# Optimization experiments

Hardware: AMD Instinct MI355X
Metric: run time of the kernel (lower is better)

## Reference

```python
import jax, jax.numpy as jnp
import numpy as np

N = 64          # Hilbert space dim
B = 4096        # batch of density matrices
K = 2           # number of jump operators
DT = 0.01       # time step
C = (0.0, 0.5, 1.0)
A = ((0.0, 0.0, 0.0), (0.5, 0.0, 0.0), (0.0, 1.0, 0.0))
BW = (1.0 / 6.0, 2.0 / 3.0, 1.0 / 6.0)
NEUMANN_ORDER = 2


def _dag(M):
    # real-valued reference: dagger == transpose on last two axes
    return jnp.swapaxes(M, -1, -2)


def _sandwich(M, rho):
    # M rho M^dag ; M:[N,N], rho:[B,N,N]
    return M @ rho @ _dag(M)


def _dissipator(L, rho):
    # sum_k L_k rho L_k^dag ; L:[K,N,N], rho:[B,N,N]
    return jnp.einsum('kij,bjl,kml->bim', L, rho, L)


def _neumann_ratio(Ui, Uj, I):
    # U(ci) U(cj)^{-1} with U(cj)^{-1} ~ sum_{p<=order} (I - U(cj))^p
    W = I - Uj
    inv = I
    Wp = I
    for _ in range(NEUMANN_ORDER):
        Wp = Wp @ W
        inv = inv + Wp
    return Ui @ inv


def _forward(rho0, U_half, U_one, L0, Lh, L1):
    I = jnp.eye(N, dtype=rho0.dtype)
    Umap = {0.0: I, 0.5: U_half, 1.0: U_one}
    Lmap = {0.0: L0, 0.5: Lh, 1.0: L1}

    def ratio(ci, cj):
        if ci == cj:
            return I
        if cj == 0.0:
            return Umap[ci]
        return _neumann_ratio(Umap[ci], Umap[cj], I)

    # intermediate stages rho^(i)
    stages = []
    for i, ci in enumerate(C):
        rho_i = rho0 if ci == 0.0 else _sandwich(Umap[ci], rho0)
        for j in range(i):
            a_ij = A[i][j]
            if a_ij == 0.0:
                continue
            cj = C[j]
            P_ij = ratio(ci, cj)
            rho_i = rho_i + DT * a_ij * _sandwich(P_ij, _dissipator(Lmap[cj], stages[j]))
        stages.append(rho_i)

    # output combination
    rho_new = _sandwich(Umap[1.0], rho0)
    for i, bi in enumerate(BW):
        if bi == 0.0:
            continue
        ci = C[i]
        Q_i = ratio(1.0, ci)
        rho_new = rho_new + DT * bi * _sandwich(Q_i, _dissipator(Lmap[ci], stages[i]))
    return rho_new


def setup_inputs() -> dict:
    key = jax.random.key(0)
    k1, k2, k3, k4, k5, k6 = jax.random.split(key, 6)
    I = jnp.eye(N, dtype=jnp.float32)
    rho0 = jax.random.normal(k1, (B, N, N), dtype=jnp.float32)
    rho0 = 0.5 * (rho0 + jnp.swapaxes(rho0, -1, -2))  # hermitian-like
    # no-jump propagators: near-identity so the Neumann series is sane
    U_half = I + 0.02 * jax.random.normal(k2, (N, N), dtype=jnp.float32)
    U_one = I + 0.04 * jax.random.normal(k3, (N, N), dtype=jnp.float32)
    L0 = 0.1 * jax.random.normal(k4, (K, N, N), dtype=jnp.float32)
    Lh = 0.1 * jax.random.normal(k5, (K, N, N), dtype=jnp.float32)
    L1 = 0.1 * jax.random.normal(k6, (K, N, N), dtype=jnp.float32)
    return {"rho0": rho0, "U_half": U_half, "U_one": U_one,
            "L0": L0, "Lh": Lh, "L1": L1}


def reference(rho0, U_half, U_one, L0, Lh, L1):
    return _forward(rho0, U_half, U_one, L0, Lh, L1)
```

## Files before the change

kernel.cpp:

```cpp
#include <hip/hip_runtime.h>
#include <hip/hip_bf16.h>

#define NDIM 64
#define BP   72
#define DT_  0.01f

typedef __attribute__((ext_vector_type(8)))  short bf16x8;
typedef __attribute__((ext_vector_type(16))) float f32x16;

struct Frag { bf16x8 f[4]; };


__device__ __forceinline__ unsigned short f2b(float x) {
    __hip_bfloat16 h = __float2bfloat16(x);
    return __builtin_bit_cast(unsigned short, h);
}
__device__ __forceinline__ float b2f(unsigned short u) {
    unsigned int v = (unsigned int)u << 16;
    return __builtin_bit_cast(float, v);
}
__device__ __forceinline__ unsigned int f2b2(float lo, float hi) {
    return (unsigned int)f2b(lo) | ((unsigned int)f2b(hi) << 16);
}


__device__ __forceinline__ bf16x8 ldfrag(const unsigned short* M, int rb, int j, int ln, int hq) {
    return *(const bf16x8*)&M[(rb + ln) * BP + j * 16 + hq * 8];
}

__device__ __forceinline__ void ldg_op(Frag& F, const unsigned short* __restrict__ p,
                                       int ln, int hq, int cw) {
#pragma unroll
    for (int j = 0; j < 4; ++j)
        F.f[j] = *(const bf16x8*)&p[(cw + ln) * 64 + j * 16 + hq * 8];
}

__device__ __forceinline__ void ldWfrag(Frag& F, const float* __restrict__ Uh,
                                        int ln, int hq, int cw) {
    const int n = cw + ln;
#pragma unroll
    for (int j = 0; j < 4; ++j) {
        const int k0 = j * 16 + hq * 8;
        const float* q = &Uh[n * 64 + k0];
        float4 u = *(const float4*)q;
        float4 v = *(const float4*)(q + 4);
        float wv[8] = {-u.x, -u.y, -u.z, -u.w, -v.x, -v.y, -v.z, -v.w};
#pragma unroll
        for (int e = 0; e < 8; ++e)
            if (n == k0 + e) wv[e] += 1.f;
        uint4 o;
        o.x = f2b2(wv[0], wv[1]); o.y = f2b2(wv[2], wv[3]);
        o.z = f2b2(wv[4], wv[5]); o.w = f2b2(wv[6], wv[7]);
        F.f[j] = __builtin_bit_cast(bf16x8, o);
    }
}

template <bool ACC>
__device__ __forceinline__ void ntg(const unsigned short* A, const Frag& F, f32x16& acc,
                                    int ln, int hq, int rb) {
    if (!ACC) {
#pragma unroll
        for (int r = 0; r < 16; ++r) acc[r] = 0.f;
    }
#pragma unroll
    for (int j = 0; j < 4; ++j)
        acc = __builtin_amdgcn_mfma_f32_32x32x16_bf16(ldfrag(A, rb, j, ln, hq), F.f[j], acc, 0, 0, 0);
}

__device__ __forceinline__ void ntg2(const unsigned short* A, const Frag& Fa, const Frag& Fb,
                                     f32x16& c0, f32x16& c1, int ln, int hq, int rb) {
#pragma unroll
    for (int r = 0; r < 16; ++r) { c0[r] = 0.f; c1[r] = 0.f; }
#pragma unroll
    for (int j = 0; j < 4; ++j) {
        bf16x8 a = ldfrag(A, rb, j, ln, hq);
        c0 = __builtin_amdgcn_mfma_f32_32x32x16_bf16(a, Fa.f[j], c0, 0, 0, 0);
        c1 = __builtin_amdgcn_mfma_f32_32x32x16_bf16(a, Fb.f[j], c1, 0, 0, 0);
    }
}

__device__ __forceinline__ void stT(unsigned short* D, const f32x16& v,
                                    int ln, int hq, int rw, int cw) {
#pragma unroll
    for (int g = 0; g < 4; ++g) {
        uint2 o;
        o.x = f2b2(v[4 * g + 0], v[4 * g + 1]);
        o.y = f2b2(v[4 * g + 2], v[4 * g + 3]);
        *(uint2*)&D[(cw + ln) * BP + rw + 8 * g + 4 * hq] = o;
    }
}

__device__ __forceinline__ void ldT(float* r, const unsigned short* S,
                                    int ln, int hq, int rw, int cw) {
#pragma unroll
    for (int g = 0; g < 4; ++g) {
        uint2 u = *(const uint2*)&S[(cw + ln) * BP + rw + 8 * g + 4 * hq];
        unsigned short o[4];
        *(uint2*)o = u;
#pragma unroll
        for (int j = 0; j < 4; ++j) r[4 * g + j] = b2f(o[j]);
    }
}


__global__ void __launch_bounds__(256) krk_setup(const float* __restrict__ Uh,
                                                 const float* __restrict__ U1,
                                                 const float* __restrict__ L0,
                                                 const float* __restrict__ Lh,
                                                 const float* __restrict__ L1,
                                                 unsigned short* __restrict__ ws) {
    __shared__ unsigned short sW [NDIM * BP];
    __shared__ unsigned short sWt[NDIM * BP];

    const int blk = blockIdx.x, tid = threadIdx.x;

    if (blk < 8) {
        const float* srcs[8] = {Uh, U1, L0, L0 + 4096, Lh, Lh + 4096, L1, L1 + 4096};
        const float* s = srcs[blk];
        unsigned short* d = ws + blk * 4096;
#pragma unroll
        for (int i = 0; i < 4; ++i) {
            int flat = (tid + i * 256) * 4;
            float4 v = *(const float4*)&s[flat];
            uint2 o; o.x = f2b2(v.x, v.y); o.y = f2b2(v.z, v.w);
            *(uint2*)&d[flat] = o;
        }
        return;
    }

    const int lane = tid & 63, w = tid >> 6, ln = lane & 31, hq = lane >> 5;
    const int rw = 32 * (w >> 1), cw = 32 * (w & 1);

#pragma unroll
    for (int i = 0; i < 4; ++i) {
        int flat = (tid + i * 256) * 4;
        int r = flat >> 6, c = flat & 63;
        float4 u = *(const float4*)&Uh[flat];
        float wv[4] = {-u.x, -u.y, -u.z, -u.w};
#pragma unroll
        for (int j = 0; j < 4; ++j)
            if (r == c + j) wv[j] += 1.f;
        unsigned short o[4] = {f2b(wv[0]), f2b(wv[1]), f2b(wv[2]), f2b(wv[3])};
        *(uint2*)&sW[r * BP + c] = *(uint2*)o;
#pragma unroll
        for (int j = 0; j < 4; ++j) sWt[(c + j) * BP + r] = o[j];
    }
    Frag Fw;
    ldWfrag(Fw, Uh, ln, hq, cw);
    __syncthreads();

    f32x16 t0;
    ntg<false>(sWt, Fw, t0, ln, hq, rw);
    float wts[16];
    ldT(wts, sW, ln, hq, rw, cw);
    unsigned short* ws8 = ws + 8 * 4096;
#pragma unroll
    for (int g = 0; g < 4; ++g) {
        uint2 o;
        float v0, v1;
#pragma unroll
        for (int j = 0; j < 4; j += 2) {
            int r0 = 4 * g + j, r1 = r0 + 1;
            int row0 = rw + (r0 & 3) + 8 * g + 4 * hq;
            int row1 = row0 + 1;
            v0 = ((row0 == cw + ln) ? 1.f : 0.f) + wts[r0] + t0[r0];
            v1 = ((row1 == cw + ln) ? 1.f : 0.f) + wts[r1] + t0[r1];
            if (j == 0) o.x = f2b2(v0, v1); else o.y = f2b2(v0, v1);
        }
        *(uint2*)&ws8[(cw + ln) * 64 + rw + 8 * g + 4 * hq] = o;
    }
}


__global__ void __launch_bounds__(256) krk_main(const float* __restrict__ rho0,
                                                const unsigned short* __restrict__ ws,
                                                float* __restrict__ out) {
    __shared__ unsigned short B0[NDIM * BP];
    __shared__ unsigned short B1[NDIM * BP];
    __shared__ unsigned short B2[NDIM * BP];
    __shared__ unsigned short B3[NDIM * BP];

    const int tid = threadIdx.x;
    const int w = tid >> 6, lane = tid & 63, ln = lane & 31, hq = lane >> 5;
    const int rw = 32 * (w >> 1), cw = 32 * (w & 1);
    const float* rho = rho0 + (size_t)blockIdx.x * (NDIM * NDIM);

    const float c12 = 0.5f * DT_, c16 = DT_ / 6.f, c23 = 2.f * DT_ / 3.f;

    f32x16 t0, t1, s0, a1;
    Frag Fa, Fb, Fc;

#pragma unroll
    for (int i = 0; i < 4; ++i) {
        int flat = (tid + i * 256) * 4;
        int r = flat >> 6, c = flat & 63;
        float4 v = *(const float4*)&rho[flat];
        uint2 o; o.x = f2b2(v.x, v.y); o.y = f2b2(v.z, v.w);
        *(uint2*)&B0[r * BP + c] = o;
    }
    ldg_op(Fa, ws + 2 * 4096, ln, hq, cw);
    ldg_op(Fb, ws + 3 * 4096, ln, hq, cw);
    __syncthreads();

    ntg2(B0, Fa, Fb, t0, t1, ln, hq, rw);
    stT(B1, t0, ln, hq, rw, cw);
    stT(B2, t1, ln, hq, rw, cw);
    __syncthreads();

    ntg<false>(B1, Fa, s0, ln, hq, rw);
    ntg<true >(B2, Fb, s0, ln, hq, rw);
    {
        float r0s[16];
        ldT(r0s, B0, ln, hq, rw, cw);
        f32x16 X;
#pragma unroll
        for (int r = 0; r < 16; ++r) X[r] = r0s[r] + c12 * s0[r];
        stT(B0, X, ln, hq, rw, cw);
    }
    ldg_op(Fc, ws + 0 * 4096, ln, hq, cw);
    __syncthreads();

    ntg<false>(B0, Fc, t0, ln, hq, rw);
    stT(B3, t0, ln, hq, rw, cw);
    __syncthreads();

    ntg<false>(B3, Fc, t0, ln, hq, rw);
    stT(B1, t0, ln, hq, rw, cw);
    ldg_op(Fa, ws + 4 * 4096, ln, hq, cw);
    ldg_op(Fb, ws + 5 * 4096, ln, hq, cw);
    __syncthreads();

    ntg2(B1, Fa, Fb, t0, t1, ln, hq, rw);
    stT(B2, t0, ln, hq, rw, cw);
    stT(B3, t1, ln, hq, rw, cw);
    __syncthreads();

    ntg<false>(B2, Fa, t0, ln, hq, rw);
    ntg<true >(B3, Fb, t0, ln, hq, rw);
    stT(B1, t0, ln, hq, rw, cw);
    ldg_op(Fc, ws + 8 * 4096, ln, hq, cw);
    __syncthreads();

    ntg<false>(B1, Fc, t0, ln, hq, rw);
    stT(B2, t0, ln, hq, rw, cw);
    __syncthreads();

    {
        f32x16 h1;
        ntg<false>(B2, Fc, h1, ln, hq, rw);
        float xs[16];
        ldT(xs, B0, ln, hq, rw, cw);
        f32x16 M1, M2;
#pragma unroll
        for (int r = 0; r < 16; ++r) {
            M1[r] = xs[r] + (c16 - c12) * s0[r] + c23 * h1[r];
            M2[r] = xs[r] - c12 * s0[r] + DT_ * h1[r];
        }
        stT(B1, M1, ln, hq, rw, cw);
        stT(B3, M2, ln, hq, rw, cw);
    }
    ldg_op(Fc, ws + 1 * 4096, ln, hq, cw);
    __syncthreads();

    ntg<false>(B1, Fc, t0, ln, hq, rw);
    stT(B0, t0, ln, hq, rw, cw);
    ntg<false>(B3, Fc, t1, ln, hq, rw);
    stT(B2, t1, ln, hq, rw, cw);
    __syncthreads();

    ntg<false>(B0, Fc, a1, ln, hq, rw);
    ntg<false>(B2, Fc, t0, ln, hq, rw);
    stT(B1, t0, ln, hq, rw, cw);
    ldg_op(Fa, ws + 6 * 4096, ln, hq, cw);
    ldg_op(Fb, ws + 7 * 4096, ln, hq, cw);
    __syncthreads();

    ntg2(B1, Fa, Fb, t0, t1, ln, hq, rw);
    stT(B0, t0, ln, hq, rw, cw);
    stT(B2, t1, ln, hq, rw, cw);
    __syncthreads();

    ntg<false>(B0, Fa, t0, ln, hq, rw);
    ntg<true >(B2, Fb, t0, ln, hq, rw);
    {
        float* o = out + (size_t)blockIdx.x * (NDIM * NDIM);
#pragma unroll
        for (int g = 0; g < 4; ++g) {
            float4 v;
            v.x = a1[4 * g + 0] + c16 * t0[4 * g + 0];
            v.y = a1[4 * g + 1] + c16 * t0[4 * g + 1];
            v.z = a1[4 * g + 2] + c16 * t0[4 * g + 2];
            v.w = a1[4 * g + 3] + c16 * t0[4 * g + 3];
            *(float4*)&o[(cw + ln) * 64 + rw + 8 * g + 4 * hq] = v;
        }
    }
}


extern "C" void kernel_launch(void* const* d_in, const int* in_sizes, int n_in,
                              void* d_out, int out_size, void* d_ws, size_t ws_size,
                              hipStream_t stream) {
    const float* rho0 = (const float*)d_in[0];
    const float* Uh   = (const float*)d_in[1];
    const float* U1   = (const float*)d_in[2];
    const float* L0   = (const float*)d_in[3];
    const float* Lh   = (const float*)d_in[4];
    const float* L1   = (const float*)d_in[5];
    float* out = (float*)d_out;
    unsigned short* ws = (unsigned short*)d_ws;

    int Bn = in_sizes[0] / (NDIM * NDIM);

    krk_setup<<<9, 256, 0, stream>>>(Uh, U1, L0, Lh, L1, ws);
    krk_main<<<Bn, 256, 0, stream>>>(rho0, ws, out);
}
```

Measured before the change: 180.1 us.

## Assign one wavefront per matrix with private LDS buffers, removing block syncs

```diff
diff --git a/kernel.cpp b/kernel.cpp
--- a/kernel.cpp
+++ b/kernel.cpp
@@ -1,14 +1,15 @@
 #include <hip/hip_runtime.h>
 #include <hip/hip_bf16.h>
 
-#define NDIM 64
-#define BP   72
-#define DT_  0.01f
+#define NDIM  64
+#define BP    72
+#define SLICE (NDIM * BP)
+#define DT_   0.01f
 
 typedef __attribute__((ext_vector_type(8)))  short bf16x8;
 typedef __attribute__((ext_vector_type(16))) float f32x16;
 
-struct Frag { bf16x8 f[4]; };
+struct OpF { bf16x8 f[2][4]; };
 
 
 __device__ __forceinline__ unsigned short f2b(float x) {
@@ -24,82 +25,139 @@
 }
 
 
-__device__ __forceinline__ bf16x8 ldfrag(const unsigned short* M, int rb, int j, int ln, int hq) {
-    return *(const bf16x8*)&M[(rb + ln) * BP + j * 16 + hq * 8];
-}
-
-__device__ __forceinline__ void ldg_op(Frag& F, const unsigned short* __restrict__ p,
-                                       int ln, int hq, int cw) {
+__device__ __forceinline__ void ld_ws_op(OpF& F, const unsigned short* __restrict__ p,
+                                         int ln, int hq) {
+#pragma unroll
+    for (int rb = 0; rb < 2; ++rb)
+#pragma unroll
+        for (int j = 0; j < 4; ++j)
+            F.f[rb][j] = *(const bf16x8*)&p[(32 * rb + ln) * 64 + j * 16 + hq * 8];
+}
+
+__device__ __forceinline__ void ld_rho(OpF& F, const float* __restrict__ p, int ln, int hq) {
+#pragma unroll
+    for (int rb = 0; rb < 2; ++rb)
+#pragma unroll
+        for (int j = 0; j < 4; ++j) {
+            const float* q = &p[(32 * rb + ln) * 64 + j * 16 + hq * 8];
+            float4 u = *(const float4*)q;
+            float4 v = *(const float4*)(q + 4);
+            uint4 o;
+            o.x = f2b2(u.x, u.y); o.y = f2b2(u.z, u.w);
+            o.z = f2b2(v.x, v.y); o.w = f2b2(v.z, v.w);
+            F.f[rb][j] = __builtin_bit_cast(bf16x8, o);
+        }
+}
+
+__device__ __forceinline__ bf16x8 lfrag(const unsigned short* buf, int rb, int j, int ln, int hq) {
+    return *(const bf16x8*)&buf[(32 * rb + ln) * BP + j * 16 + hq * 8];
+}
+
+__device__ __forceinline__ void ld_lds_op(OpF& F, const unsigned short* buf, int ln, int hq) {
+#pragma unroll
+    for (int rb = 0; rb < 2; ++rb)
+#pragma unroll
+        for (int j = 0; j < 4; ++j)
+            F.f[rb][j] = lfrag(buf, rb, j, ln, hq);
+}
+
+
+template <bool ACC>
+__device__ __forceinline__ void gemmR(f32x16 (&C)[2][2], const OpF& A, const OpF& B) {
+    if (!ACC) {
+#pragma unroll
+        for (int qr = 0; qr < 2; ++qr)
+#pragma unroll
+            for (int qc = 0; qc < 2; ++qc)
+#pragma unroll
+                for (int r = 0; r < 16; ++r) C[qr][qc][r] = 0.f;
+    }
 #pragma unroll
     for (int j = 0; j < 4; ++j)
-        F.f[j] = *(const bf16x8*)&p[(cw + ln) * 64 + j * 16 + hq * 8];
-}
-
-__device__ __forceinline__ void ldWfrag(Frag& F, const float* __restrict__ Uh,
-                                        int ln, int hq, int cw) {
-    const int n = cw + ln;
+#pragma unroll
+        for (int qr = 0; qr < 2; ++qr)
+#pragma unroll
+            for (int qc = 0; qc < 2; ++qc)
+                C[qr][qc] = __builtin_amdgcn_mfma_f32_32x32x16_bf16(
+                    A.f[qr][j], B.f[qc][j], C[qr][qc], 0, 0, 0);
+}
+
+template <bool ACC>
+__device__ __forceinline__ void gemmL(f32x16 (&C)[2][2], const unsigned short* buf,
+                                      const OpF& B, int ln, int hq) {
+    if (!ACC) {
+#pragma unroll
+        for (int qr = 0; qr < 2; ++qr)
+#pragma unroll
+            for (int qc = 0; qc < 2; ++qc)
+#pragma unroll
+                for (int r = 0; r < 16; ++r) C[qr][qc][r] = 0.f;
+    }
 #pragma unroll
     for (int j = 0; j < 4; ++j) {
-        const int k0 = j * 16 + hq * 8;
-        const float* q = &Uh[n * 64 + k0];
-        float4 u = *(const float4*)q;
-        float4 v = *(const float4*)(q + 4);
-        float wv[8] = {-u.x, -u.y, -u.z, -u.w, -v.x, -v.y, -v.z, -v.w};
-#pragma unroll
-        for (int e = 0; e < 8; ++e)
-            if (n == k0 + e) wv[e] += 1.f;
-        uint4 o;
-        o.x = f2b2(wv[0], wv[1]); o.y = f2b2(wv[2], wv[3]);
-        o.z = f2b2(wv[4], wv[5]); o.w = f2b2(wv[6], wv[7]);
-        F.f[j] = __builtin_bit_cast(bf16x8, o);
-    }
-}
-
-template <bool ACC>
-__device__ __forceinline__ void ntg(const unsigned short* A, const Frag& F, f32x16& acc,
-                                    int ln, int hq, int rb) {
-    if (!ACC) {
-#pragma unroll
-        for (int r = 0; r < 16; ++r) acc[r] = 0.f;
-    }
-#pragma unroll
-    for (int j = 0; j < 4; ++j)
-        acc = __builtin_amdgcn_mfma_f32_32x32x16_bf16(ldfrag(A, rb, j, ln, hq), F.f[j], acc, 0, 0, 0);
-}
-
-__device__ __forceinline__ void ntg2(const unsigned short* A, const Frag& Fa, const Frag& Fb,
-                                     f32x16& c0, f32x16& c1, int ln, int hq, int rb) {
-#pragma unroll
-    for (int r = 0; r < 16; ++r) { c0[r] = 0.f; c1[r] = 0.f; }
-#pragma unroll
-    for (int j = 0; j < 4; ++j) {
-        bf16x8 a = ldfrag(A, rb, j, ln, hq);
-        c0 = __builtin_amdgcn_mfma_f32_32x32x16_bf16(a, Fa.f[j], c0, 0, 0, 0);
-        c1 = __builtin_amdgcn_mfma_f32_32x32x16_bf16(a, Fb.f[j], c1, 0, 0, 0);
-    }
-}
-
-__device__ __forceinline__ void stT(unsigned short* D, const f32x16& v,
-                                    int ln, int hq, int rw, int cw) {
-#pragma unroll
-    for (int g = 0; g < 4; ++g) {
-        uint2 o;
-        o.x = f2b2(v[4 * g + 0], v[4 * g + 1]);
-        o.y = f2b2(v[4 * g + 2], v[4 * g + 3]);
-        *(uint2*)&D[(cw + ln) * BP + rw + 8 * g + 4 * hq] = o;
-    }
-}
-
-__device__ __forceinline__ void ldT(float* r, const unsigned short* S,
-                                    int ln, int hq, int rw, int cw) {
-#pragma unroll
-    for (int g = 0; g < 4; ++g) {
-        uint2 u = *(const uint2*)&S[(cw + ln) * BP + rw + 8 * g + 4 * hq];
-        unsigned short o[4];
-        *(uint2*)o = u;
-#pragma unroll
-        for (int j = 0; j < 4; ++j) r[4 * g + j] = b2f(o[j]);
-    }
+        bf16x8 a0 = lfrag(buf, 0, j, ln, hq);
+        bf16x8 a1 = lfrag(buf, 1, j, ln, hq);
+        C[0][0] = __builtin_amdgcn_mfma_f32_32x32x16_bf16(a0, B.f[0][j], C[0][0], 0, 0, 0);
+        C[0][1] = __builtin_amdgcn_mfma_f32_32x32x16_bf16(a0, B.f[1][j], C[0][1], 0, 0, 0);
+        C[1][0] = __builtin_amdgcn_mfma_f32_32x32x16_bf16(a1, B.f[0][j], C[1][0], 0, 0, 0);
+        C[1][1] = __builtin_amdgcn_mfma_f32_32x32x16_bf16(a1, B.f[1][j], C[1][1], 0, 0, 0);
+    }
+}
+
+__device__ __forceinline__ void stTF(unsigned short* buf, const f32x16 (&C)[2][2],
+                                     int ln, int hq) {
+#pragma unroll
+    for (int qc = 0; qc < 2; ++qc)
+#pragma unroll
+        for (int qr = 0; qr < 2; ++qr)
+#pragma unroll
+            for (int g = 0; g < 4; ++g) {
+                uint2 o;
+                o.x = f2b2(C[qr][qc][4 * g + 0], C[qr][qc][4 * g + 1]);
+                o.y = f2b2(C[qr][qc][4 * g + 2], C[qr][qc][4 * g + 3]);
+                *(uint2*)&buf[(32 * qc + ln) * BP + 32 * qr + 8 * g + 4 * hq] = o;
+            }
+}
+
+
+__device__ __forceinline__ bf16x8 comb2(bf16x8 a, bf16x8 b, float cb) {
+    bf16x8 r;
+#pragma unroll
+    for (int e = 0; e < 8; e += 2) {
+        float f0 = b2f((unsigned short)a[e])     + cb * b2f((unsigned short)b[e]);
+        float f1 = b2f((unsigned short)a[e + 1]) + cb * b2f((unsigned short)b[e + 1]);
+        unsigned int pk = f2b2(f0, f1);
+        r[e]     = (short)(pk & 0xffffu);
+        r[e + 1] = (short)(pk >> 16);
+    }
+    return r;
+}
+__device__ __forceinline__ bf16x8 comb3(bf16x8 a, bf16x8 b, bf16x8 c, float cb, float cc) {
+    bf16x8 r;
+#pragma unroll
+    for (int e = 0; e < 8; e += 2) {
+        float f0 = b2f((unsigned short)a[e]) + cb * b2f((unsigned short)b[e])
+                 + cc * b2f((unsigned short)c[e]);
+        float f1 = b2f((unsigned short)a[e + 1]) + cb * b2f((unsigned short)b[e + 1])
+                 + cc * b2f((unsigned short)c[e + 1]);
+        unsigned int pk = f2b2(f0, f1);
+        r[e]     = (short)(pk & 0xffffu);
+        r[e + 1] = (short)(pk >> 16);
+    }
+    return r;
+}
+__device__ __forceinline__ void opComb2(OpF& R, const OpF& A, const OpF& B, float cb) {
+#pragma unroll
+    for (int rb = 0; rb < 2; ++rb)
+#pragma unroll
+        for (int j = 0; j < 4; ++j) R.f[rb][j] = comb2(A.f[rb][j], B.f[rb][j], cb);
+}
+__device__ __forceinline__ void opComb3(OpF& R, const OpF& A, const OpF& B, const OpF& Cc,
+                                        float cb, float cc) {
+#pragma unroll
+    for (int rb = 0; rb < 2; ++rb)
+#pragma unroll
+        for (int j = 0; j < 4; ++j) R.f[rb][j] = comb3(A.f[rb][j], B.f[rb][j], Cc.f[rb][j], cb, cc);
 }
 
 
@@ -113,6 +171,7 @@
     __shared__ unsigned short sWt[NDIM * BP];
 
     const int blk = blockIdx.x, tid = threadIdx.x;
+    const float c16 = DT_ / 6.f;
 
     if (blk < 8) {
         const float* srcs[8] = {Uh, U1, L0, L0 + 4096, Lh, Lh + 4096, L1, L1 + 4096};
@@ -127,6 +186,18 @@
         }
         return;
     }
+    if (blk >= 9) {
+        const float* s = (blk == 9) ? L1 : L1 + 4096;
+        unsigned short* d = ws + blk * 4096;
+#pragma unroll
+        for (int i = 0; i < 4; ++i) {
+            int flat = (tid + i * 256) * 4;
+            float4 v = *(const float4*)&s[flat];
+            uint2 o; o.x = f2b2(c16 * v.x, c16 * v.y); o.y = f2b2(c16 * v.z, c16 * v.w);
+            *(uint2*)&d[flat] = o;
+        }
+        return;
+    }
 
     const int lane = tid & 63, w = tid >> 6, ln = lane & 31, hq = lane >> 5;
     const int rw = 32 * (w >> 1), cw = 32 * (w & 1);
@@ -145,26 +216,52 @@
 #pragma unroll
         for (int j = 0; j < 4; ++j) sWt[(c + j) * BP + r] = o[j];
     }
-    Frag Fw;
-    ldWfrag(Fw, Uh, ln, hq, cw);
+    OpF Fw;
+    {
+        const int n = cw + ln;
+#pragma unroll
+        for (int j = 0; j < 4; ++j) {
+            const int k0 = j * 16 + hq * 8;
+            const float* q = &Uh[n * 64 + k0];
+            float4 u = *(const float4*)q;
+            float4 v = *(const float4*)(q + 4);
+            float wv[8] = {-u.x, -u.y, -u.z, -u.w, -v.x, -v.y, -v.z, -v.w};
+#pragma unroll
+            for (int e = 0; e < 8; ++e)
+                if (n == k0 + e) wv[e] += 1.f;
+            uint4 o;
+            o.x = f2b2(wv[0], wv[1]); o.y = f2b2(wv[2], wv[3]);
+            o.z = f2b2(wv[4], wv[5]); o.w = f2b2(wv[6], wv[7]);
+            Fw.f[0][j] = __builtin_bit_cast(bf16x8, o);
+        }
+    }
     __syncthreads();
 
     f32x16 t0;
-    ntg<false>(sWt, Fw, t0, ln, hq, rw);
+#pragma unroll
+    for (int r = 0; r < 16; ++r) t0[r] = 0.f;
+#pragma unroll
+    for (int j = 0; j < 4; ++j)
+        t0 = __builtin_amdgcn_mfma_f32_32x32x16_bf16(
+            *(const bf16x8*)&sWt[(rw + ln) * BP + j * 16 + hq * 8], Fw.f[0][j], t0, 0, 0, 0);
     float wts[16];
-    ldT(wts, sW, ln, hq, rw, cw);
+#pragma unroll
+    for (int g = 0; g < 4; ++g) {
+        uint2 u = *(const uint2*)&sW[(cw + ln) * BP + rw + 8 * g + 4 * hq];
+        unsigned short o[4]; *(uint2*)o = u;
+#pragma unroll
+        for (int j = 0; j < 4; ++j) wts[4 * g + j] = b2f(o[j]);
+    }
     unsigned short* ws8 = ws + 8 * 4096;
 #pragma unroll
     for (int g = 0; g < 4; ++g) {
         uint2 o;
-        float v0, v1;
 #pragma unroll
         for (int j = 0; j < 4; j += 2) {
             int r0 = 4 * g + j, r1 = r0 + 1;
             int row0 = rw + (r0 & 3) + 8 * g + 4 * hq;
-            int row1 = row0 + 1;
-            v0 = ((row0 == cw + ln) ? 1.f : 0.f) + wts[r0] + t0[r0];
-            v1 = ((row1 == cw + ln) ? 1.f : 0.f) + wts[r1] + t0[r1];
+            float v0 = ((row0 == cw + ln) ? 1.f : 0.f) + wts[r0] + t0[r0];
+            float v1 = ((row0 + 1 == cw + ln) ? 1.f : 0.f) + wts[r1] + t0[r1];
             if (j == 0) o.x = f2b2(v0, v1); else o.y = f2b2(v0, v1);
         }
         *(uint2*)&ws8[(cw + ln) * 64 + rw + 8 * g + 4 * hq] = o;
@@ -172,128 +269,88 @@
 }
 
 
-__global__ void __launch_bounds__(256) krk_main(const float* __restrict__ rho0,
-                                                const unsigned short* __restrict__ ws,
-                                                float* __restrict__ out) {
-    __shared__ unsigned short B0[NDIM * BP];
-    __shared__ unsigned short B1[NDIM * BP];
-    __shared__ unsigned short B2[NDIM * BP];
-    __shared__ unsigned short B3[NDIM * BP];
+__global__ void __launch_bounds__(128, 2) krk_main(const float* __restrict__ rho0,
+                                                   const unsigned short* __restrict__ ws,
+                                                   float* __restrict__ out) {
+    __shared__ unsigned short L[2 * 2 * SLICE];
 
     const int tid = threadIdx.x;
-    const int w = tid >> 6, lane = tid & 63, ln = lane & 31, hq = lane >> 5;
-    const int rw = 32 * (w >> 1), cw = 32 * (w & 1);
-    const float* rho = rho0 + (size_t)blockIdx.x * (NDIM * NDIM);
+    const int wv = tid >> 6, lane = tid & 63, ln = lane & 31, hq = lane >> 5;
+    unsigned short* bufA = &L[(2 * wv + 0) * SLICE];
+    unsigned short* bufB = &L[(2 * wv + 1) * SLICE];
+    const int mat = blockIdx.x * 2 + wv;
+    const float* rho = rho0 + (size_t)mat * (NDIM * NDIM);
 
     const float c12 = 0.5f * DT_, c16 = DT_ / 6.f, c23 = 2.f * DT_ / 3.f;
 
-    f32x16 t0, t1, s0, a1;
-    Frag Fa, Fb, Fc;
-
-#pragma unroll
-    for (int i = 0; i < 4; ++i) {
-        int flat = (tid + i * 256) * 4;
-        int r = flat >> 6, c = flat & 63;
-        float4 v = *(const float4*)&rho[flat];
-        uint2 o; o.x = f2b2(v.x, v.y); o.y = f2b2(v.z, v.w);
-        *(uint2*)&B0[r * BP + c] = o;
-    }
-    ldg_op(Fa, ws + 2 * 4096, ln, hq, cw);
-    ldg_op(Fb, ws + 3 * 4096, ln, hq, cw);
-    __syncthreads();
-
-    ntg2(B0, Fa, Fb, t0, t1, ln, hq, rw);
-    stT(B1, t0, ln, hq, rw, cw);
-    stT(B2, t1, ln, hq, rw, cw);
-    __syncthreads();
-
-    ntg<false>(B1, Fa, s0, ln, hq, rw);
-    ntg<true >(B2, Fb, s0, ln, hq, rw);
-    {
-        float r0s[16];
-        ldT(r0s, B0, ln, hq, rw, cw);
-        f32x16 X;
-#pragma unroll
-        for (int r = 0; r < 16; ++r) X[r] = r0s[r] + c12 * s0[r];
-        stT(B0, X, ln, hq, rw, cw);
-    }
-    ldg_op(Fc, ws + 0 * 4096, ln, hq, cw);
-    __syncthreads();
-
-    ntg<false>(B0, Fc, t0, ln, hq, rw);
-    stT(B3, t0, ln, hq, rw, cw);
-    __syncthreads();
-
-    ntg<false>(B3, Fc, t0, ln, hq, rw);
-    stT(B1, t0, ln, hq, rw, cw);
-    ldg_op(Fa, ws + 4 * 4096, ln, hq, cw);
-    ldg_op(Fb, ws + 5 * 4096, ln, hq, cw);
-    __syncthreads();
-
-    ntg2(B1, Fa, Fb, t0, t1, ln, hq, rw);
-    stT(B2, t0, ln, hq, rw, cw);
-    stT(B3, t1, ln, hq, rw, cw);
-    __syncthreads();
-
-    ntg<false>(B2, Fa, t0, ln, hq, rw);
-    ntg<true >(B3, Fb, t0, ln, hq, rw);
-    stT(B1, t0, ln, hq, rw, cw);
-    ldg_op(Fc, ws + 8 * 4096, ln, hq, cw);
-    __syncthreads();
-
-    ntg<false>(B1, Fc, t0, ln, hq, rw);
-    stT(B2, t0, ln, hq, rw, cw);
-    __syncthreads();
-
-    {
-        f32x16 h1;
-        ntg<false>(B2, Fc, h1, ln, hq, rw);
-        float xs[16];
-        ldT(xs, B0, ln, hq, rw, cw);
-        f32x16 M1, M2;
-#pragma unroll
-        for (int r = 0; r < 16; ++r) {
-            M1[r] = xs[r] + (c16 - c12) * s0[r] + c23 * h1[r];
-            M2[r] = xs[r] - c12 * s0[r] + DT_ * h1[r];
-        }
-        stT(B1, M1, ln, hq, rw, cw);
-        stT(B3, M2, ln, hq, rw, cw);
-    }
-    ldg_op(Fc, ws + 1 * 4096, ln, hq, cw);
-    __syncthreads();
-
-    ntg<false>(B1, Fc, t0, ln, hq, rw);
-    stT(B0, t0, ln, hq, rw, cw);
-    ntg<false>(B3, Fc, t1, ln, hq, rw);
-    stT(B2, t1, ln, hq, rw, cw);
-    __syncthreads();
-
-    ntg<false>(B0, Fc, a1, ln, hq, rw);
-    ntg<false>(B2, Fc, t0, ln, hq, rw);
-    stT(B1, t0, ln, hq, rw, cw);
-    ldg_op(Fa, ws + 6 * 4096, ln, hq, cw);
-    ldg_op(Fb, ws + 7 * 4096, ln, hq, cw);
-    __syncthreads();
-
-    ntg2(B1, Fa, Fb, t0, t1, ln, hq, rw);
-    stT(B0, t0, ln, hq, rw, cw);
-    stT(B2, t1, ln, hq, rw, cw);
-    __syncthreads();
-
-    ntg<false>(B0, Fa, t0, ln, hq, rw);
-    ntg<true >(B2, Fb, t0, ln, hq, rw);
-    {
-        float* o = out + (size_t)blockIdx.x * (NDIM * NDIM);
-#pragma unroll
-        for (int g = 0; g < 4; ++g) {
-            float4 v;
-            v.x = a1[4 * g + 0] + c16 * t0[4 * g + 0];
-            v.y = a1[4 * g + 1] + c16 * t0[4 * g + 1];
-            v.z = a1[4 * g + 2] + c16 * t0[4 * g + 2];
-            v.w = a1[4 * g + 3] + c16 * t0[4 * g + 3];
-            *(float4*)&o[(cw + ln) * 64 + rw + 8 * g + 4 * hq] = v;
-        }
-    }
+    OpF Rf, S0f, H1f, Oa, Ob, Tf;
+    f32x16 C[2][2];
+
+    ld_rho(Rf, rho, ln, hq);
+    ld_ws_op(Oa, ws + 2 * 4096, ln, hq);
+    ld_ws_op(Ob, ws + 3 * 4096, ln, hq);
+
+    gemmR<false>(C, Rf, Oa); stTF(bufA, C, ln, hq);
+    gemmR<false>(C, Rf, Ob); stTF(bufB, C, ln, hq);
+    gemmL<false>(C, bufA, Oa, ln, hq);
+    gemmL<true >(C, bufB, Ob, ln, hq);
+    stTF(bufA, C, ln, hq);
+    ld_lds_op(S0f, bufA, ln, hq);
+
+    opComb2(Tf, Rf, S0f, c12);
+    ld_ws_op(Oa, ws + 0 * 4096, ln, hq);
+    gemmR<false>(C, Tf, Oa); stTF(bufA, C, ln, hq);
+    gemmL<false>(C, bufA, Oa, ln, hq);
+    stTF(bufB, C, ln, hq);
+
+    ld_ws_op(Oa, ws + 4 * 4096, ln, hq);
+    ld_ws_op(Ob, ws + 5 * 4096, ln, hq);
+    gemmL<false>(C, bufB, Oa, ln, hq); stTF(bufA, C, ln, hq);
+    gemmL<false>(C, bufB, Ob, ln, hq); stTF(bufB, C, ln, hq);
+    gemmL<false>(C, bufA, Oa, ln, hq);
+    gemmL<true >(C, bufB, Ob, ln, hq);
+    stTF(bufA, C, ln, hq);
+
+    ld_ws_op(Oa, ws + 8 * 4096, ln, hq);
+    gemmL<false>(C, bufA, Oa, ln, hq); stTF(bufB, C, ln, hq);
+    gemmL<false>(C, bufB, Oa, ln, hq);
+    stTF(bufA, C, ln, hq);
+    ld_lds_op(H1f, bufA, ln, hq);
+
+    OpF M1f, M2f;
+    opComb3(M1f, Rf, S0f, H1f, c16, c23);
+    opComb2(M2f, Rf, H1f, DT_);
+    ld_ws_op(Oa, ws + 1 * 4096, ln, hq);
+    gemmR<false>(C, M1f, Oa); stTF(bufA, C, ln, hq);
+    gemmR<false>(C, M2f, Oa); stTF(bufB, C, ln, hq);
+    gemmL<false>(C, bufB, Oa, ln, hq);
+    stTF(bufB, C, ln, hq);
+
+    f32x16 O[2][2];
+    gemmL<false>(O, bufA, Oa, ln, hq);
+    ld_ws_op(Oa, ws + 6 * 4096, ln, hq);
+    ld_ws_op(Ob, ws + 7 * 4096, ln, hq);
+    gemmL<false>(C, bufB, Oa, ln, hq); stTF(bufA, C, ln, hq);
+    gemmL<false>(C, bufB, Ob, ln, hq); stTF(bufB, C, ln, hq);
+    ld_ws_op(Oa, ws + 9 * 4096, ln, hq);
+    ld_ws_op(Ob, ws + 10 * 4096, ln, hq);
+    gemmL<true>(O, bufA, Oa, ln, hq);
+    gemmL<true>(O, bufB, Ob, ln, hq);
+
+    float* o = out + (size_t)mat * (NDIM * NDIM);
+#pragma unroll
+    for (int qc = 0; qc < 2; ++qc)
+#pragma unroll
+        for (int qr = 0; qr < 2; ++qr)
+#pragma unroll
+            for (int g = 0; g < 4; ++g) {
+                float4 v;
+                v.x = O[qr][qc][4 * g + 0];
+                v.y = O[qr][qc][4 * g + 1];
+                v.z = O[qr][qc][4 * g + 2];
+                v.w = O[qr][qc][4 * g + 3];
+                *(float4*)&o[(32 * qc + ln) * 64 + 32 * qr + 8 * g + 4 * hq] = v;
+            }
 }
 
 
@@ -311,6 +368,6 @@
 
     int Bn = in_sizes[0] / (NDIM * NDIM);
 
-    krk_setup<<<9, 256, 0, stream>>>(Uh, U1, L0, Lh, L1, ws);
-    krk_main<<<Bn, 256, 0, stream>>>(rho0, ws, out);
-}
+    krk_setup<<<11, 256, 0, stream>>>(Uh, U1, L0, Lh, L1, ws);
+    krk_main<<<Bn / 2, 128, 0, stream>>>(rho0, ws, out);
+}
```

After: 192.7 us. 1.07x slower.
